# Optimization experiments

Measured on AMD Instinct MI355X. Metric: run time of the kernel, lower is better.

The kernel has to match this reference:

```python
import jax, jax.numpy as jnp
import numpy as np

B, S, F = 4096, 2048, 4


def setup_inputs() -> dict:
    key = jax.random.key(0)
    k1, k2 = jax.random.split(key)
    x = jax.random.normal(k1, (B, S, F), dtype=jnp.float32)
    # context_weight initialized ~ N(1, 0.05) in the original
    context_weight = 1.0 + 0.05 * jax.random.normal(k2, (F, 1), dtype=jnp.float32)
    context_bias = jnp.zeros((1,), dtype=jnp.float32)  # frozen at zero (requires_grad=False)
    return {"x": x, "context_weight": context_weight, "context_bias": context_bias}


def reference(x, context_weight, context_bias):
    # batch_matrix_mul: per-doc mm with [F,1] weight + bias + tanh, squeezed -> [B, S]
    scores = jnp.tanh(jnp.einsum('bsf,fo->bs', x, context_weight) + context_bias[0])
    # zero_gating_softmax_normalize: zero scores (padding) get zero attention weight
    mask = (scores != 0).astype(scores.dtype)            # [B, S]
    m = jnp.max(scores, axis=-1, keepdims=True)          # stable shift (math-equivalent)
    e = jnp.exp(scores - m) * mask                       # [B, S]
    attn = e / jnp.sum(e, axis=-1, keepdims=True)
    return attn
```

## Files before the change

### kernel.cpp

```cpp
#include <hip/hip_runtime.h>
#include <math.h>


#define S_LEN 2048
#define BLOCK 256
#define PER_THREAD (S_LEN / BLOCK)

__device__ __forceinline__ float fast_tanh(float z) {
    z = fminf(fmaxf(z, -20.0f), 20.0f);
    const float t2 = __expf(2.0f * z);
    return (t2 - 1.0f) * __builtin_amdgcn_rcpf(t2 + 1.0f);
}

__global__ __launch_bounds__(BLOCK) void sent_att_kernel(
    const float* __restrict__ x,
    const float* __restrict__ w,
    const float* __restrict__ bias,
    float* __restrict__ out)
{
    const int b = blockIdx.x;
    const int t = threadIdx.x;
    const float4* __restrict__ xrow =
        reinterpret_cast<const float4*>(x) + (size_t)b * S_LEN;

    const float w0 = w[0], w1 = w[1], w2 = w[2], w3 = w[3];
    const float cb = bias[0];

    float e[PER_THREAD];
    float lsum = 0.0f;
#pragma unroll
    for (int k = 0; k < PER_THREAD; ++k) {
        const int s = t + k * BLOCK;
        const float4 v = xrow[s];
        const float z = v.x * w0 + v.y * w1 + v.z * w2 + v.w * w3 + cb;
        const float sv = fast_tanh(z);
        const float ev = (sv != 0.0f) ? __expf(sv) : 0.0f;
        e[k] = ev;
        lsum += ev;
    }

#pragma unroll
    for (int off = 32; off > 0; off >>= 1)
        lsum += __shfl_xor(lsum, off, 64);

    __shared__ float ssum[BLOCK / 64];
    const int wave = t >> 6;
    const int lane = t & 63;
    if (lane == 0) ssum[wave] = lsum;
    __syncthreads();
    const float total = ssum[0] + ssum[1] + ssum[2] + ssum[3];
    const float inv = 1.0f / total;

    float* __restrict__ orow = out + (size_t)b * S_LEN;
#pragma unroll
    for (int k = 0; k < PER_THREAD; ++k)
        orow[t + k * BLOCK] = e[k] * inv;
}

extern "C" void kernel_launch(void* const* d_in, const int* in_sizes, int n_in,
                              void* d_out, int out_size, void* d_ws, size_t ws_size,
                              hipStream_t stream) {
    const float* x    = (const float*)d_in[0];
    const float* w    = (const float*)d_in[1];
    const float* bias = (const float*)d_in[2];
    float* out = (float*)d_out;

    const int B = in_sizes[0] / (S_LEN * 4);
    sent_att_kernel<<<B, BLOCK, 0, stream>>>(x, w, bias, out);
}
```

Before: 29.27 us.

## Map one wavefront per row and use nontemporal loads and stores

Each wavefront now owns a whole row of 2048 elements instead of one 256-thread block per row, so the sum reduction needs only wave shuffles and no shared memory or __syncthreads. Global loads and stores become nontemporal to avoid polluting the cache on this streaming workload. In exchange each lane keeps 32 values in registers instead of 8, which raises register pressure and can lower occupancy. Each lane also issues four times as many loads.

```diff
diff --git a/kernel.cpp b/kernel.cpp
--- a/kernel.cpp
+++ b/kernel.cpp
@@ -3,8 +3,11 @@
 
 
 #define S_LEN 2048
-#define BLOCK 256
-#define PER_THREAD (S_LEN / BLOCK)
+#define WAVES_PER_BLOCK 4
+#define BLOCK (WAVES_PER_BLOCK * 64)
+#define PER_LANE (S_LEN / 64)
+
+typedef float floatv4 __attribute__((ext_vector_type(4)));
 
 __device__ __forceinline__ float fast_tanh(float z) {
     z = fminf(fmaxf(z, -20.0f), 20.0f);
@@ -12,26 +15,27 @@
     return (t2 - 1.0f) * __builtin_amdgcn_rcpf(t2 + 1.0f);
 }
 
-__global__ __launch_bounds__(BLOCK) void sent_att_kernel(
+__global__ __launch_bounds__(BLOCK, 4) void sent_att_kernel(
     const float* __restrict__ x,
     const float* __restrict__ w,
     const float* __restrict__ bias,
     float* __restrict__ out)
 {
-    const int b = blockIdx.x;
-    const int t = threadIdx.x;
-    const float4* __restrict__ xrow =
-        reinterpret_cast<const float4*>(x) + (size_t)b * S_LEN;
+    const int wave = threadIdx.x >> 6;
+    const int lane = threadIdx.x & 63;
+    const int b = blockIdx.x * WAVES_PER_BLOCK + wave;
+
+    const floatv4* __restrict__ xrow =
+        reinterpret_cast<const floatv4*>(x) + (size_t)b * S_LEN;
 
     const float w0 = w[0], w1 = w[1], w2 = w[2], w3 = w[3];
     const float cb = bias[0];
 
-    float e[PER_THREAD];
+    float e[PER_LANE];
     float lsum = 0.0f;
 #pragma unroll
-    for (int k = 0; k < PER_THREAD; ++k) {
-        const int s = t + k * BLOCK;
-        const float4 v = xrow[s];
+    for (int k = 0; k < PER_LANE; ++k) {
+        const floatv4 v = __builtin_nontemporal_load(&xrow[lane + k * 64]);
         const float z = v.x * w0 + v.y * w1 + v.z * w2 + v.w * w3 + cb;
         const float sv = fast_tanh(z);
         const float ev = (sv != 0.0f) ? __expf(sv) : 0.0f;
@@ -42,19 +46,12 @@
 #pragma unroll
     for (int off = 32; off > 0; off >>= 1)
         lsum += __shfl_xor(lsum, off, 64);
-
-    __shared__ float ssum[BLOCK / 64];
-    const int wave = t >> 6;
-    const int lane = t & 63;
-    if (lane == 0) ssum[wave] = lsum;
-    __syncthreads();
-    const float total = ssum[0] + ssum[1] + ssum[2] + ssum[3];
-    const float inv = 1.0f / total;
+    const float inv = 1.0f / lsum;
 
     float* __restrict__ orow = out + (size_t)b * S_LEN;
 #pragma unroll
-    for (int k = 0; k < PER_THREAD; ++k)
-        orow[t + k * BLOCK] = e[k] * inv;
+    for (int k = 0; k < PER_LANE; ++k)
+        __builtin_nontemporal_store(e[k] * inv, &orow[lane + k * 64]);
 }
 
 extern "C" void kernel_launch(void* const* d_in, const int* in_sizes, int n_in,
@@ -66,5 +63,5 @@
     float* out = (float*)d_out;
 
     const int B = in_sizes[0] / (S_LEN * 4);
-    sent_att_kernel<<<B, BLOCK, 0, stream>>>(x, w, bias, out);
+    sent_att_kernel<<<B / WAVES_PER_BLOCK, BLOCK, 0, stream>>>(x, w, bias, out);
 }
```

Result: slower. 31.01 us (+6.0%).
